# Performance work log

Measured on AMD Instinct MI355X. Metric: run time of the kernel, lower is better.

Reference implementation:

```python
import jax, jax.numpy as jnp
import numpy as np

N_NODES = 100000
N_EDGES = 1600000
IN_DIM = 64
HID_DIM = 128
OUT_DIM = 128


def setup_inputs() -> dict:
    key = jax.random.key(0)
    ks = jax.random.split(key, 12)
    s = 0.05
    return {
        "x": jax.random.normal(ks[0], (N_NODES, IN_DIM), jnp.float32),
        "edge_index": jax.random.randint(ks[1], (2, N_EDGES), 0, N_NODES, jnp.int64),
        "edge_attr": jax.random.uniform(ks[2], (N_EDGES, 2), jnp.float32),
        # conv1 MLP: Linear(IN+2, HID) -> ReLU -> Linear(HID, HID)
        "W11": jax.random.normal(ks[3], (IN_DIM + 2, HID_DIM), jnp.float32) * s,
        "b11": jax.random.normal(ks[4], (HID_DIM,), jnp.float32) * s,
        "W12": jax.random.normal(ks[5], (HID_DIM, HID_DIM), jnp.float32) * s,
        "b12": jax.random.normal(ks[6], (HID_DIM,), jnp.float32) * s,
        # conv2 MLP: Linear(HID+2, OUT) -> ReLU -> Linear(OUT, OUT)
        "W21": jax.random.normal(ks[7], (HID_DIM + 2, OUT_DIM), jnp.float32) * s,
        "b21": jax.random.normal(ks[8], (OUT_DIM,), jnp.float32) * s,
        "W22": jax.random.normal(ks[9], (OUT_DIM, OUT_DIM), jnp.float32) * s,
        "b22": jax.random.normal(ks[10], (OUT_DIM,), jnp.float32) * s,
    }


def _gin_conv(x, edge_index, edge_attr, W1, b1, W2, b2):
    N = x.shape[0]
    loop = jnp.arange(N, dtype=edge_index.dtype)
    src = jnp.concatenate([edge_index[0], loop])  # [E+N] message sources
    dst = jnp.concatenate([edge_index[1], loop])  # [E+N] aggregation targets
    # self-loop edge_attr filled with 1.0 (PyG add_self_loops default)
    ea = jnp.concatenate([edge_attr, jnp.ones((N, edge_attr.shape[1]), edge_attr.dtype)], axis=0)
    m = jnp.concatenate([x[src], ea], axis=-1)  # [E+N, F+2] gather + concat
    h = jnp.dot(jax.nn.relu(jnp.dot(m, W1) + b1), W2) + b2  # edge MLP
    return jax.ops.segment_sum(h, dst, num_segments=N)  # scatter-add aggregate


def reference(x, edge_index, edge_attr, W11, b11, W12, b12, W21, b21, W22, b22):
    h = _gin_conv(x, edge_index, edge_attr, W11, b11, W12, b12)
    h = jax.nn.relu(h)
    return _gin_conv(h, edge_index, edge_attr, W21, b21, W22, b22)
```

## Files before the change

### kernel.cpp

```cpp
#include <hip/hip_runtime.h>


typedef unsigned int uint;
typedef __attribute__((ext_vector_type(8))) short bf16x8;
typedef __attribute__((ext_vector_type(4))) float f32x4;

#define BSHIFT 9
#define BNODES (1 << BSHIFT)

static __device__ __forceinline__ unsigned short f2bf(float f) {
    uint u = __float_as_uint(f);
    uint r = (u + 0x7fffu + ((u >> 16) & 1u)) >> 16;
    return (unsigned short)r;
}


__global__ void wprep_all(const float* __restrict__ W11, const float* __restrict__ W12,
                          const float* __restrict__ W21, const float* __restrict__ W22,
                          unsigned short* Wt11, unsigned short* Wt12,
                          unsigned short* Wt21, unsigned short* Wt22,
                          int* bcnt, int* ptr, int N, int E) {
    int idx = blockIdx.x * 256 + threadIdx.x;
    if (idx < 256) bcnt[idx] = 0;
    if (idx == 0) ptr[N] = E;
    const float* W; unsigned short* Wt; int K; int off;
    if (idx < 64 * 128)        { W = W11; Wt = Wt11; K = 64;  off = idx; }
    else if (idx < 192 * 128)  { W = W12; Wt = Wt12; K = 128; off = idx - 64 * 128; }
    else if (idx < 320 * 128)  { W = W21; Wt = Wt21; K = 128; off = idx - 192 * 128; }
    else if (idx < 448 * 128)  { W = W22; Wt = Wt22; K = 128; off = idx - 320 * 128; }
    else return;
    int k = off >> 7, n = off & 127;
    Wt[n * K + k] = f2bf(W[k * 128 + n]);
}


__global__ __launch_bounds__(512) void bin_kernel(
    const int* __restrict__ src, const int* __restrict__ dst,
    const float* __restrict__ ea, int* __restrict__ bcnt,
    int2* __restrict__ barr, int CAP, int E, int B) {
    __shared__ int hist[256];
    __shared__ int bbase[256];
    __shared__ int gbase[256];
    __shared__ int wtot[4];
    __shared__ int2 sorted[4096];
    __shared__ unsigned char bof[4096];
    const int tileBase = blockIdx.x * 4096;
    int n = E - tileBase; if (n > 4096) n = 4096; if (n <= 0) return;
    const int tid = threadIdx.x;
    const int lane = tid & 63;
    if (tid < 256) hist[tid] = 0;
    __syncthreads();

    int2 ent[8]; int bk[8]; int rk[8];
#pragma unroll
    for (int kk = 0; kk < 8; kk++) {
        int i = kk * 512 + tid;
        bk[kk] = -1;
        if (i < n) {
            int e = tileBase + i;
            int s = src[e], d = dst[e];
            float2 a = reinterpret_cast<const float2*>(ea)[e];
            int b = d >> BSHIFT;
            int dloc = d & (BNODES - 1);
            ent[kk].x = s | (dloc << 17);
            ent[kk].y = (int)((uint)f2bf(a.x) | ((uint)f2bf(a.y) << 16));
            bk[kk] = b;
            rk[kk] = atomicAdd(&hist[b], 1);
        }
    }
    __syncthreads();
    int hv = (tid < 256) ? hist[tid] : 0;
    int inc = hv;
#pragma unroll
    for (int off = 1; off < 64; off <<= 1) {
        int tt = __shfl_up(inc, off, 64);
        if (lane >= off) inc += tt;
    }
    if ((tid >> 6) < 4 && lane == 63) wtot[tid >> 6] = inc;
    __syncthreads();
    if (tid == 0) { int run = 0; for (int i = 0; i < 4; i++) { int tt = wtot[i]; wtot[i] = run; run += tt; } }
    __syncthreads();
    if (tid < 256) bbase[tid] = inc - hv + wtot[tid >> 6];
    if (tid < B && hist[tid] > 0) gbase[tid] = atomicAdd(&bcnt[tid], hist[tid]);
    __syncthreads();
#pragma unroll
    for (int kk = 0; kk < 8; kk++) {
        if (bk[kk] >= 0) {
            int p = bbase[bk[kk]] + rk[kk];
            sorted[p] = ent[kk];
            bof[p] = (unsigned char)bk[kk];
        }
    }
    __syncthreads();
    for (int i = tid; i < n; i += 512) {
        int b = bof[i];
        barr[(long)b * CAP + gbase[b] + (i - bbase[b])] = sorted[i];
    }
}


static __device__ void csr_body(const int2* __restrict__ barr, const int* __restrict__ bcnt,
                                int CAP, int N, int2* __restrict__ csr, int* __restrict__ ptr) {
    __shared__ int hist[BNODES];
    __shared__ int lptr[BNODES];
    __shared__ int wtot[8];
    __shared__ int sbase;
    const int g = blockIdx.x;
    const int tid = threadIdx.x;
    const int lane = tid & 63;
    const int cnt = bcnt[g];
    if (tid == 0) sbase = 0;
    hist[tid] = 0;
    __syncthreads();
    if (tid < g) atomicAdd(&sbase, bcnt[tid]);
    const int2* my = barr + (long)g * CAP;
    for (int i = tid; i < cnt; i += 512)
        atomicAdd(&hist[((uint)my[i].x) >> 17], 1);
    __syncthreads();
    int v = hist[tid];
    int inc = v;
#pragma unroll
    for (int off = 1; off < 64; off <<= 1) {
        int tt = __shfl_up(inc, off, 64);
        if (lane >= off) inc += tt;
    }
    if (lane == 63) wtot[tid >> 6] = inc;
    __syncthreads();
    if (tid == 0) { int run = 0; for (int i = 0; i < 8; i++) { int tt = wtot[i]; wtot[i] = run; run += tt; } }
    __syncthreads();
    const int base = sbase;
    int excl = inc - v + wtot[tid >> 6];
    lptr[tid] = excl;
    int gnode = g * BNODES + tid;
    if (gnode < N) ptr[gnode] = base + excl;
    __syncthreads();
    for (int i = tid; i < cnt; i += 512) {
        int2 e = my[i];
        int pos = base + atomicAdd(&lptr[((uint)e.x) >> 17], 1);
        int2 o; o.x = e.x & 0x1FFFF; o.y = e.y;
        csr[pos] = o;
    }
}


template <int K, bool IN_F32, bool OUT_BF16, bool USE_CNT, bool RELU>
static __device__ __forceinline__ void gemm_body(
    const void* __restrict__ Ain, const unsigned short* __restrict__ Wt,
    const float* __restrict__ bias, const int* __restrict__ ptr,
    void* __restrict__ Cout, int N, int tid, long rowBase) {
    constexpr int KS = K / 32;
    const int wave = tid >> 6;
    const int lane = tid & 63;
    const int m = lane & 15, quad = lane >> 4;

    bf16x8 bfrag[2][KS];
#pragma unroll
    for (int ct = 0; ct < 2; ct++) {
        int col = (wave * 2 + ct) * 16 + m;
#pragma unroll
        for (int ks = 0; ks < KS; ks++)
            bfrag[ct][ks] = *(const bf16x8*)(Wt + (long)col * K + ks * 32 + quad * 8);
    }

#pragma unroll
    for (int rt = 0; rt < 4; rt++) {
        long row = rowBase + rt * 16 + m;
        long rc = row < N ? row : (long)N - 1;
        bf16x8 afrag[KS];
        if (IN_F32) {
            const float* arow = (const float*)Ain + rc * K;
#pragma unroll
            for (int ks = 0; ks < KS; ks++) {
                float4 lo = *(const float4*)(arow + ks * 32 + quad * 8);
                float4 hi = *(const float4*)(arow + ks * 32 + quad * 8 + 4);
                bf16x8 f;
                f[0] = (short)f2bf(lo.x); f[1] = (short)f2bf(lo.y);
                f[2] = (short)f2bf(lo.z); f[3] = (short)f2bf(lo.w);
                f[4] = (short)f2bf(hi.x); f[5] = (short)f2bf(hi.y);
                f[6] = (short)f2bf(hi.z); f[7] = (short)f2bf(hi.w);
                afrag[ks] = f;
            }
        } else {
            const unsigned short* arow = (const unsigned short*)Ain + rc * K;
#pragma unroll
            for (int ks = 0; ks < KS; ks++)
                afrag[ks] = *(const bf16x8*)(arow + ks * 32 + quad * 8);
        }

#pragma unroll
        for (int ct = 0; ct < 2; ct++) {
            f32x4 acc = {0.f, 0.f, 0.f, 0.f};
#pragma unroll
            for (int ks = 0; ks < KS; ks++)
                acc = __builtin_amdgcn_mfma_f32_16x16x32_bf16(afrag[ks], bfrag[ct][ks], acc, 0, 0, 0);

            int col = (wave * 2 + ct) * 16 + m;
            float b = bias[col];
#pragma unroll
            for (int r = 0; r < 4; r++) {
                long orow = rowBase + rt * 16 + quad * 4 + r;
                if (orow < N) {
                    float v = acc[r];
                    if (USE_CNT) v += b * (float)(ptr[orow + 1] - ptr[orow] + 1);
                    else v += b;
                    if (RELU) v = fmaxf(v, 0.f);
                    if (OUT_BF16) ((unsigned short*)Cout)[orow * 128 + col] = f2bf(v);
                    else ((float*)Cout)[orow * 128 + col] = v;
                }
            }
        }
    }
}


__global__ __launch_bounds__(512) void csr_gemm1(
    const int2* __restrict__ barr, const int* __restrict__ bcnt, int CAP, int N,
    int2* __restrict__ csr, int* __restrict__ ptr, int CSRB,
    const float* __restrict__ x, const unsigned short* __restrict__ Wt11,
    const float* __restrict__ b11, unsigned short* __restrict__ A_bf) {
    if ((int)blockIdx.x < CSRB) {
        csr_body(barr, bcnt, CAP, N, csr, ptr);
    } else {
        int bid = blockIdx.x - CSRB;
        int sub = threadIdx.x >> 8;
        gemm_body<64, true, true, false, false>(x, Wt11, b11, nullptr, A_bf, N,
                                                threadIdx.x & 255,
                                                (long)bid * 128 + sub * 64);
    }
}


static __device__ __forceinline__ void gather_lds(
    const uint* __restrict__ Au, const int* __restrict__ ptr,
    const int2* __restrict__ csr, const float* __restrict__ we,
    uint* __restrict__ ts_u, int N, int tid, int rowBase) {
    const int w = tid >> 6;
    const int t = tid & 63;
    const int c = 2 * t;
    const float w0x = we[c], w0y = we[c + 1];
    const float w1x = we[128 + c], w1y = we[128 + c + 1];
    const char* Ab = (const char*)Au;
    const uint t4 = (uint)t * 4u;
#define LD(sidx) (*(const uint*)(Ab + ((((uint)(sidx)) << 8) + t4)))
#define ACC(rv, ev)                                                      \
    {                                                                    \
        float a0 = __uint_as_float(((uint)(ev)) << 16);                  \
        float a1 = __uint_as_float(((uint)(ev)) & 0xffff0000u);          \
        float vx = __uint_as_float((rv) << 16);                          \
        float vy = __uint_as_float((rv) & 0xffff0000u);                  \
        vx = fmaf(a0, w0x, fmaf(a1, w1x, vx));                           \
        vy = fmaf(a0, w0y, fmaf(a1, w1y, vy));                           \
        ax += fmaxf(vx, 0.f);                                            \
        ay += fmaxf(vy, 0.f);                                            \
    }
#define EDGE(i, off)                                                     \
    int2 c##i = csr[k + (off)];                                          \
    uint s##i = (uint)__builtin_amdgcn_readfirstlane(c##i.x);            \
    uint e##i = (uint)__builtin_amdgcn_readfirstlane(c##i.y);

    for (int i = 0; i < 16; i++) {
        int node = rowBase + w * 16 + i;
        if (node >= N) break;

        uint selfv = LD((uint)node);
        float ax = fmaxf(__uint_as_float(selfv << 16) + w0x + w1x, 0.f);
        float ay = fmaxf(__uint_as_float(selfv & 0xffff0000u) + w0y + w1y, 0.f);

        int k   = __builtin_amdgcn_readfirstlane(ptr[node]);
        int end = __builtin_amdgcn_readfirstlane(ptr[node + 1]);

        for (; k + 8 <= end; k += 8) {
            EDGE(0, 0) EDGE(1, 1) EDGE(2, 2) EDGE(3, 3)
            EDGE(4, 4) EDGE(5, 5) EDGE(6, 6) EDGE(7, 7)
            uint r0 = LD(s0); uint r1 = LD(s1); uint r2 = LD(s2); uint r3 = LD(s3);
            uint r4 = LD(s4); uint r5 = LD(s5); uint r6 = LD(s6); uint r7 = LD(s7);
            ACC(r0, e0) ACC(r1, e1) ACC(r2, e2) ACC(r3, e3)
            ACC(r4, e4) ACC(r5, e5) ACC(r6, e6) ACC(r7, e7)
        }
        for (; k + 4 <= end; k += 4) {
            EDGE(0, 0) EDGE(1, 1) EDGE(2, 2) EDGE(3, 3)
            uint r0 = LD(s0); uint r1 = LD(s1); uint r2 = LD(s2); uint r3 = LD(s3);
            ACC(r0, e0) ACC(r1, e1) ACC(r2, e2) ACC(r3, e3)
        }
        for (; k < end; k++) {
            EDGE(0, 0)
            uint r0 = LD(s0);
            ACC(r0, e0)
        }
        ts_u[(w * 16 + i) * 68 + t] = (uint)f2bf(ax) | ((uint)f2bf(ay) << 16);
    }
#undef EDGE
#undef ACC
#undef LD
}


__global__ __launch_bounds__(256, 4) void gather_mid(
    const uint* __restrict__ Au, const int* __restrict__ ptr,
    const int2* __restrict__ csr, const float* __restrict__ we,
    const unsigned short* __restrict__ WtA, const float* __restrict__ biasA,
    const unsigned short* __restrict__ WtB, const float* __restrict__ biasB,
    unsigned short* __restrict__ Cout, int N) {
    __shared__ uint ts_u[64 * 68];
    unsigned short* ts = (unsigned short*)ts_u;
    const int tid = threadIdx.x;
    const int rowBase = blockIdx.x * 64;

    gather_lds(Au, ptr, csr, we, ts_u, N, tid, rowBase);
    __syncthreads();

    const int wave = tid >> 6, lane = tid & 63;
    const int m = lane & 15, quad = lane >> 4;

    bf16x8 bfrag[2][4];
#pragma unroll
    for (int ct = 0; ct < 2; ct++) {
        int col = (wave * 2 + ct) * 16 + m;
#pragma unroll
        for (int ks = 0; ks < 4; ks++)
            bfrag[ct][ks] = *(const bf16x8*)(WtA + (long)col * 128 + ks * 32 + quad * 8);
    }

    f32x4 acc[4][2];
#pragma unroll
    for (int rt = 0; rt < 4; rt++) {
        const unsigned short* lr = ts + (rt * 16 + m) * 136;
        bf16x8 af[4];
#pragma unroll
        for (int ks = 0; ks < 4; ks++)
            af[ks] = *(const bf16x8*)(lr + ks * 32 + quad * 8);
#pragma unroll
        for (int ct = 0; ct < 2; ct++) {
            f32x4 a = {0.f, 0.f, 0.f, 0.f};
#pragma unroll
            for (int ks = 0; ks < 4; ks++)
                a = __builtin_amdgcn_mfma_f32_16x16x32_bf16(af[ks], bfrag[ct][ks], a, 0, 0, 0);
            acc[rt][ct] = a;
        }
    }
    __syncthreads();

#pragma unroll
    for (int rt = 0; rt < 4; rt++) {
        float cntf[4];
#pragma unroll
        for (int r = 0; r < 4; r++) {
            long grow = rowBase + rt * 16 + quad * 4 + r;
            cntf[r] = (grow < N) ? (float)(ptr[grow + 1] - ptr[grow] + 1) : 1.f;
        }
#pragma unroll
        for (int ct = 0; ct < 2; ct++) {
            int col = (wave * 2 + ct) * 16 + m;
            float b = biasA[col];
#pragma unroll
            for (int r = 0; r < 4; r++) {
                int row = rt * 16 + quad * 4 + r;
                ts[row * 136 + col] = f2bf(fmaxf(acc[rt][ct][r] + b * cntf[r], 0.f));
            }
        }
    }
    __syncthreads();

#pragma unroll
    for (int ct = 0; ct < 2; ct++) {
        int col = (wave * 2 + ct) * 16 + m;
#pragma unroll
        for (int ks = 0; ks < 4; ks++)
            bfrag[ct][ks] = *(const bf16x8*)(WtB + (long)col * 128 + ks * 32 + quad * 8);
    }
#pragma unroll
    for (int rt = 0; rt < 4; rt++) {
        const unsigned short* lr = ts + (rt * 16 + m) * 136;
        bf16x8 af[4];
#pragma unroll
        for (int ks = 0; ks < 4; ks++)
            af[ks] = *(const bf16x8*)(lr + ks * 32 + quad * 8);
#pragma unroll
        for (int ct = 0; ct < 2; ct++) {
            f32x4 a = {0.f, 0.f, 0.f, 0.f};
#pragma unroll
            for (int ks = 0; ks < 4; ks++)
                a = __builtin_amdgcn_mfma_f32_16x16x32_bf16(af[ks], bfrag[ct][ks], a, 0, 0, 0);
            int col = (wave * 2 + ct) * 16 + m;
            float b = biasB[col];
#pragma unroll
            for (int r = 0; r < 4; r++) {
                long grow = rowBase + rt * 16 + quad * 4 + r;
                if (grow < N) Cout[grow * 128 + col] = f2bf(a[r] + b);
            }
        }
    }
}


__global__ __launch_bounds__(256, 4) void gather_out(
    const uint* __restrict__ Au, const int* __restrict__ ptr,
    const int2* __restrict__ csr, const float* __restrict__ we,
    const unsigned short* __restrict__ Wt, const float* __restrict__ bias,
    float* __restrict__ out, int N) {
    __shared__ uint ts_u[64 * 68];
    unsigned short* ts = (unsigned short*)ts_u;
    const int tid = threadIdx.x;
    const int rowBase = blockIdx.x * 64;

    gather_lds(Au, ptr, csr, we, ts_u, N, tid, rowBase);
    __syncthreads();

    const int wave = tid >> 6, lane = tid & 63;
    const int m = lane & 15, quad = lane >> 4;

    bf16x8 bfrag[2][4];
#pragma unroll
    for (int ct = 0; ct < 2; ct++) {
        int col = (wave * 2 + ct) * 16 + m;
#pragma unroll
        for (int ks = 0; ks < 4; ks++)
            bfrag[ct][ks] = *(const bf16x8*)(Wt + (long)col * 128 + ks * 32 + quad * 8);
    }

#pragma unroll
    for (int rt = 0; rt < 4; rt++) {
        const unsigned short* lr = ts + (rt * 16 + m) * 136;
        bf16x8 af[4];
#pragma unroll
        for (int ks = 0; ks < 4; ks++)
            af[ks] = *(const bf16x8*)(lr + ks * 32 + quad * 8);
#pragma unroll
        for (int ct = 0; ct < 2; ct++) {
            f32x4 a = {0.f, 0.f, 0.f, 0.f};
#pragma unroll
            for (int ks = 0; ks < 4; ks++)
                a = __builtin_amdgcn_mfma_f32_16x16x32_bf16(af[ks], bfrag[ct][ks], a, 0, 0, 0);
            int col = (wave * 2 + ct) * 16 + m;
            float b = bias[col];
#pragma unroll
            for (int r = 0; r < 4; r++) {
                long grow = rowBase + rt * 16 + quad * 4 + r;
                if (grow < N) {
                    float cnt = (float)(ptr[grow + 1] - ptr[grow] + 1);
                    out[grow * 128 + col] = a[r] + b * cnt;
                }
            }
        }
    }
}


extern "C" void kernel_launch(void* const* d_in, const int* in_sizes, int n_in,
                              void* d_out, int out_size, void* d_ws, size_t ws_size,
                              hipStream_t stream) {
    const float* x   = (const float*)d_in[0];
    const int*   ei  = (const int*)d_in[1];
    const float* ea  = (const float*)d_in[2];
    const float* W11 = (const float*)d_in[3];
    const float* b11 = (const float*)d_in[4];
    const float* W12 = (const float*)d_in[5];
    const float* b12 = (const float*)d_in[6];
    const float* W21 = (const float*)d_in[7];
    const float* b21 = (const float*)d_in[8];
    const float* W22 = (const float*)d_in[9];
    const float* b22 = (const float*)d_in[10];
    float* out = (float*)d_out;

    const int N = in_sizes[0] / 64;
    const int E = in_sizes[1] / 2;
    const int* src = ei;
    const int* dst = ei + E;

    const int B = (N + BNODES - 1) >> BSHIFT;
    const int CAP = E / B + 4096;

    char* p = (char*)d_ws;
    unsigned short* A_bf = (unsigned short*)p;  p += (size_t)N * 128 * 2;
    unsigned short* A2_bf = (unsigned short*)p;
    int2* barr = (int2*)A2_bf;                  p += (size_t)N * 128 * 2;
    int2* csr  = (int2*)p;                      p += (size_t)E * 8;
    int* ptr   = (int*)p;                       p += (size_t)(N + 1) * 4;
    int* bcnt  = (int*)p;                       p += 256 * 4;
    unsigned short* Wt11 = (unsigned short*)p;  p += (size_t)64 * 128 * 2;
    unsigned short* Wt12 = (unsigned short*)p;  p += (size_t)128 * 128 * 2;
    unsigned short* Wt21 = (unsigned short*)p;  p += (size_t)128 * 128 * 2;
    unsigned short* Wt22 = (unsigned short*)p;

    const int binBlocks = (E + 4095) / 4096;
    const int tileBlocks = (N + 63) / 64;
    const int g1Tiles = (N + 127) / 128;

    wprep_all<<<224, 256, 0, stream>>>(W11, W12, W21, W22,
                                       Wt11, Wt12, Wt21, Wt22,
                                       bcnt, ptr, N, E);
    bin_kernel<<<binBlocks, 512, 0, stream>>>(src, dst, ea, bcnt, barr, CAP, E, B);
    csr_gemm1<<<B + g1Tiles, 512, 0, stream>>>(barr, bcnt, CAP, N, csr, ptr, B,
                                               x, Wt11, b11, A_bf);
    gather_mid<<<tileBlocks, 256, 0, stream>>>((const uint*)A_bf, ptr, csr,
                                               W11 + 64 * 128, Wt12, b12, Wt21, b21,
                                               A2_bf, N);
    gather_out<<<tileBlocks, 256, 0, stream>>>((const uint*)A2_bf, ptr, csr,
                                               W21 + 128 * 128, Wt22, b22, out, N);
}
```

Before: 347.3 us.

## Fuse weight prep into binning, interleave two-node gathers, drop occupancy hints

The weight-transpose kernel is merged into the binning kernel as extra blocks, and the bcnt zeroing moves to a hipMemsetAsync. The gather loop now processes two nodes at once with interleaved 4-edge batches, which raises memory-level parallelism, though the 8-edge unroll is gone. The __launch_bounds__ occupancy hint of 4 is removed from the gather kernels. The output kernel hoists the degree counts out of the column loop and uses nontemporal stores. Dropping the occupancy hint may raise register use and lower the number of resident waves.

```diff
diff --git a/kernel.cpp b/kernel.cpp
--- a/kernel.cpp
+++ b/kernel.cpp
@@ -2,52 +2,55 @@
 
 
 typedef unsigned int uint;
+typedef unsigned short ushort;
 typedef __attribute__((ext_vector_type(8))) short bf16x8;
 typedef __attribute__((ext_vector_type(4))) float f32x4;
 
 #define BSHIFT 9
 #define BNODES (1 << BSHIFT)
 
-static __device__ __forceinline__ unsigned short f2bf(float f) {
+static __device__ __forceinline__ ushort f2bf(float f) {
     uint u = __float_as_uint(f);
     uint r = (u + 0x7fffu + ((u >> 16) & 1u)) >> 16;
-    return (unsigned short)r;
-}
-
-
-__global__ void wprep_all(const float* __restrict__ W11, const float* __restrict__ W12,
-                          const float* __restrict__ W21, const float* __restrict__ W22,
-                          unsigned short* Wt11, unsigned short* Wt12,
-                          unsigned short* Wt21, unsigned short* Wt22,
-                          int* bcnt, int* ptr, int N, int E) {
-    int idx = blockIdx.x * 256 + threadIdx.x;
-    if (idx < 256) bcnt[idx] = 0;
-    if (idx == 0) ptr[N] = E;
-    const float* W; unsigned short* Wt; int K; int off;
-    if (idx < 64 * 128)        { W = W11; Wt = Wt11; K = 64;  off = idx; }
-    else if (idx < 192 * 128)  { W = W12; Wt = Wt12; K = 128; off = idx - 64 * 128; }
-    else if (idx < 320 * 128)  { W = W21; Wt = Wt21; K = 128; off = idx - 192 * 128; }
-    else if (idx < 448 * 128)  { W = W22; Wt = Wt22; K = 128; off = idx - 320 * 128; }
-    else return;
-    int k = off >> 7, n = off & 127;
-    Wt[n * K + k] = f2bf(W[k * 128 + n]);
-}
-
-
-__global__ __launch_bounds__(512) void bin_kernel(
+    return (ushort)r;
+}
+static __device__ __forceinline__ int rfl(int v) { return __builtin_amdgcn_readfirstlane(v); }
+
+
+__global__ __launch_bounds__(512) void wprep_bin(
+    const float* __restrict__ W11, const float* __restrict__ W12,
+    const float* __restrict__ W21, const float* __restrict__ W22,
+    ushort* Wt11, ushort* Wt12, ushort* Wt21, ushort* Wt22,
     const int* __restrict__ src, const int* __restrict__ dst,
     const float* __restrict__ ea, int* __restrict__ bcnt,
-    int2* __restrict__ barr, int CAP, int E, int B) {
+    int2* __restrict__ barr, int CAP, int N, int E, int B, int WB,
+    int* __restrict__ ptr) {
     __shared__ int hist[256];
     __shared__ int bbase[256];
     __shared__ int gbase[256];
     __shared__ int wtot[4];
     __shared__ int2 sorted[4096];
     __shared__ unsigned char bof[4096];
-    const int tileBase = blockIdx.x * 4096;
-    int n = E - tileBase; if (n > 4096) n = 4096; if (n <= 0) return;
     const int tid = threadIdx.x;
     const int lane = tid & 63;
+
+    if ((int)blockIdx.x < WB) {
+        int idx = blockIdx.x * 512 + tid;
+        if (idx == 0) ptr[N] = E;
+        if (idx < 448 * 128) {
+            const float* W; ushort* Wt; int K; int off;
+            if (idx < 64 * 128)        { W = W11; Wt = Wt11; K = 64;  off = idx; }
+            else if (idx < 192 * 128)  { W = W12; Wt = Wt12; K = 128; off = idx - 64 * 128; }
+            else if (idx < 320 * 128)  { W = W21; Wt = Wt21; K = 128; off = idx - 192 * 128; }
+            else                       { W = W22; Wt = Wt22; K = 128; off = idx - 320 * 128; }
+            int k = off >> 7, n = off & 127;
+            Wt[n * K + k] = f2bf(W[k * 128 + n]);
+        }
+        return;
+    }
+
+    const int tileBase = ((int)blockIdx.x - WB) * 4096;
+    int n = E - tileBase; if (n > 4096) n = 4096; if (n <= 0) return;
     if (tid < 256) hist[tid] = 0;
     __syncthreads();
 
@@ -81,7 +84,7 @@
     if (tid == 0) { int run = 0; for (int i = 0; i < 4; i++) { int tt = wtot[i]; wtot[i] = run; run += tt; } }
     __syncthreads();
     if (tid < 256) bbase[tid] = inc - hv + wtot[tid >> 6];
-    if (tid < B && hist[tid] > 0) gbase[tid] = atomicAdd(&bcnt[tid], hist[tid]);
+    if (tid < B && hv > 0) gbase[tid] = atomicAdd(&bcnt[tid], hv);
     __syncthreads();
 #pragma unroll
     for (int kk = 0; kk < 8; kk++) {
@@ -143,9 +146,9 @@
 }
 
 
-template <int K, bool IN_F32, bool OUT_BF16, bool USE_CNT, bool RELU>
+template <int K, bool IN_F32, bool OUT_BF16, bool USE_CNT>
 static __device__ __forceinline__ void gemm_body(
-    const void* __restrict__ Ain, const unsigned short* __restrict__ Wt,
+    const void* __restrict__ Ain, const ushort* __restrict__ Wt,
     const float* __restrict__ bias, const int* __restrict__ ptr,
     void* __restrict__ Cout, int N, int tid, long rowBase) {
     constexpr int KS = K / 32;
@@ -181,7 +184,7 @@
                 afrag[ks] = f;
             }
         } else {
-            const unsigned short* arow = (const unsigned short*)Ain + rc * K;
+            const ushort* arow = (const ushort*)Ain + rc * K;
 #pragma unroll
             for (int ks = 0; ks < KS; ks++)
                 afrag[ks] = *(const bf16x8*)(arow + ks * 32 + quad * 8);
@@ -203,8 +206,7 @@
                     float v = acc[r];
                     if (USE_CNT) v += b * (float)(ptr[orow + 1] - ptr[orow] + 1);
                     else v += b;
-                    if (RELU) v = fmaxf(v, 0.f);
-                    if (OUT_BF16) ((unsigned short*)Cout)[orow * 128 + col] = f2bf(v);
+                    if (OUT_BF16) ((ushort*)Cout)[orow * 128 + col] = f2bf(v);
                     else ((float*)Cout)[orow * 128 + col] = v;
                 }
             }
@@ -216,19 +218,58 @@
 __global__ __launch_bounds__(512) void csr_gemm1(
     const int2* __restrict__ barr, const int* __restrict__ bcnt, int CAP, int N,
     int2* __restrict__ csr, int* __restrict__ ptr, int CSRB,
-    const float* __restrict__ x, const unsigned short* __restrict__ Wt11,
-    const float* __restrict__ b11, unsigned short* __restrict__ A_bf) {
+    const float* __restrict__ x, const ushort* __restrict__ Wt11,
+    const float* __restrict__ b11, ushort* __restrict__ A_bf) {
     if ((int)blockIdx.x < CSRB) {
         csr_body(barr, bcnt, CAP, N, csr, ptr);
     } else {
         int bid = blockIdx.x - CSRB;
         int sub = threadIdx.x >> 8;
-        gemm_body<64, true, true, false, false>(x, Wt11, b11, nullptr, A_bf, N,
-                                                threadIdx.x & 255,
-                                                (long)bid * 128 + sub * 64);
-    }
-}
-
+        gemm_body<64, true, true, false>(x, Wt11, b11, nullptr, A_bf, N,
+                                         threadIdx.x & 255,
+                                         (long)bid * 128 + sub * 64);
+    }
+}
+
+
+static __device__ __forceinline__ uint ldrow(const char* Ab, uint t4, uint sidx) {
+    return *(const uint*)(Ab + ((sidx << 8) + t4));
+}
+static __device__ __forceinline__ void accum_edge(
+    uint rv, uint ev, float w0x, float w0y, float w1x, float w1y,
+    float& ax, float& ay) {
+    float a0 = __uint_as_float(ev << 16);
+    float a1 = __uint_as_float(ev & 0xffff0000u);
+    float vx = __uint_as_float(rv << 16);
+    float vy = __uint_as_float(rv & 0xffff0000u);
+    vx = fmaf(a0, w0x, fmaf(a1, w1x, vx));
+    vy = fmaf(a0, w0y, fmaf(a1, w1y, vy));
+    ax += fmaxf(vx, 0.f);
+    ay += fmaxf(vy, 0.f);
+}
+static __device__ __forceinline__ void drain_node(
+    const char* Ab, uint t4, const int2* __restrict__ csr, int k, int end,
+    float w0x, float w0y, float w1x, float w1y, float& ax, float& ay) {
+    for (; k + 4 <= end; k += 4) {
+        int2 c0 = csr[k], c1 = csr[k + 1], c2 = csr[k + 2], c3 = csr[k + 3];
+        uint s0 = (uint)rfl(c0.x), e0 = (uint)rfl(c0.y);
+        uint s1 = (uint)rfl(c1.x), e1 = (uint)rfl(c1.y);
+        uint s2 = (uint)rfl(c2.x), e2 = (uint)rfl(c2.y);
+        uint s3 = (uint)rfl(c3.x), e3 = (uint)rfl(c3.y);
+        uint r0 = ldrow(Ab, t4, s0), r1 = ldrow(Ab, t4, s1);
+        uint r2 = ldrow(Ab, t4, s2), r3 = ldrow(Ab, t4, s3);
+        accum_edge(r0, e0, w0x, w0y, w1x, w1y, ax, ay);
+        accum_edge(r1, e1, w0x, w0y, w1x, w1y, ax, ay);
+        accum_edge(r2, e2, w0x, w0y, w1x, w1y, ax, ay);
+        accum_edge(r3, e3, w0x, w0y, w1x, w1y, ax, ay);
+    }
+    for (; k < end; k++) {
+        int2 c0 = csr[k];
+        uint s0 = (uint)rfl(c0.x), e0 = (uint)rfl(c0.y);
+        uint r0 = ldrow(Ab, t4, s0);
+        accum_edge(r0, e0, w0x, w0y, w1x, w1y, ax, ay);
+    }
+}
 
 static __device__ __forceinline__ void gather_lds(
     const uint* __restrict__ Au, const int* __restrict__ ptr,
@@ -241,68 +282,72 @@
     const float w1x = we[128 + c], w1y = we[128 + c + 1];
     const char* Ab = (const char*)Au;
     const uint t4 = (uint)t * 4u;
-#define LD(sidx) (*(const uint*)(Ab + ((((uint)(sidx)) << 8) + t4)))
-#define ACC(rv, ev)                                                      \
-    {                                                                    \
-        float a0 = __uint_as_float(((uint)(ev)) << 16);                  \
-        float a1 = __uint_as_float(((uint)(ev)) & 0xffff0000u);          \
-        float vx = __uint_as_float((rv) << 16);                          \
-        float vy = __uint_as_float((rv) & 0xffff0000u);                  \
-        vx = fmaf(a0, w0x, fmaf(a1, w1x, vx));                           \
-        vy = fmaf(a0, w0y, fmaf(a1, w1y, vy));                           \
-        ax += fmaxf(vx, 0.f);                                            \
-        ay += fmaxf(vy, 0.f);                                            \
-    }
-#define EDGE(i, off)                                                     \
-    int2 c##i = csr[k + (off)];                                          \
-    uint s##i = (uint)__builtin_amdgcn_readfirstlane(c##i.x);            \
-    uint e##i = (uint)__builtin_amdgcn_readfirstlane(c##i.y);
-
-    for (int i = 0; i < 16; i++) {
-        int node = rowBase + w * 16 + i;
-        if (node >= N) break;
-
-        uint selfv = LD((uint)node);
-        float ax = fmaxf(__uint_as_float(selfv << 16) + w0x + w1x, 0.f);
-        float ay = fmaxf(__uint_as_float(selfv & 0xffff0000u) + w0y + w1y, 0.f);
-
-        int k   = __builtin_amdgcn_readfirstlane(ptr[node]);
-        int end = __builtin_amdgcn_readfirstlane(ptr[node + 1]);
-
-        for (; k + 8 <= end; k += 8) {
-            EDGE(0, 0) EDGE(1, 1) EDGE(2, 2) EDGE(3, 3)
-            EDGE(4, 4) EDGE(5, 5) EDGE(6, 6) EDGE(7, 7)
-            uint r0 = LD(s0); uint r1 = LD(s1); uint r2 = LD(s2); uint r3 = LD(s3);
-            uint r4 = LD(s4); uint r5 = LD(s5); uint r6 = LD(s6); uint r7 = LD(s7);
-            ACC(r0, e0) ACC(r1, e1) ACC(r2, e2) ACC(r3, e3)
-            ACC(r4, e4) ACC(r5, e5) ACC(r6, e6) ACC(r7, e7)
-        }
-        for (; k + 4 <= end; k += 4) {
-            EDGE(0, 0) EDGE(1, 1) EDGE(2, 2) EDGE(3, 3)
-            uint r0 = LD(s0); uint r1 = LD(s1); uint r2 = LD(s2); uint r3 = LD(s3);
-            ACC(r0, e0) ACC(r1, e1) ACC(r2, e2) ACC(r3, e3)
-        }
-        for (; k < end; k++) {
-            EDGE(0, 0)
-            uint r0 = LD(s0);
-            ACC(r0, e0)
-        }
-        ts_u[(w * 16 + i) * 68 + t] = (uint)f2bf(ax) | ((uint)f2bf(ay) << 16);
-    }
-#undef EDGE
-#undef ACC
-#undef LD
-}
-
-
-__global__ __launch_bounds__(256, 4) void gather_mid(
+    const int nodeBase = rowBase + w * 16;
+    if (nodeBase >= N) return;
+    int kNext = rfl(ptr[nodeBase]);
+
+    for (int i = 0; i < 16; i += 2) {
+        const int n0 = nodeBase + i;
+        if (n0 >= N) break;
+        const int n1 = n0 + 1;
+        const bool h1 = (n1 < N);
+        int k0 = kNext;
+        int e0 = rfl(ptr[n0 + 1]);
+        int k1 = e0, e1 = e0;
+        if (h1) { e1 = rfl(ptr[n1 + 1]); kNext = e1; }
+
+        uint sv0 = ldrow(Ab, t4, (uint)n0);
+        float ax0 = fmaxf(__uint_as_float(sv0 << 16) + w0x + w1x, 0.f);
+        float ay0 = fmaxf(__uint_as_float(sv0 & 0xffff0000u) + w0y + w1y, 0.f);
+        float ax1 = 0.f, ay1 = 0.f;
+        if (h1) {
+            uint sv1 = ldrow(Ab, t4, (uint)n1);
+            ax1 = fmaxf(__uint_as_float(sv1 << 16) + w0x + w1x, 0.f);
+            ay1 = fmaxf(__uint_as_float(sv1 & 0xffff0000u) + w0y + w1y, 0.f);
+        }
+        while (k0 + 4 <= e0 && k1 + 4 <= e1) {
+            int2 ca0 = csr[k0], ca1 = csr[k0 + 1], ca2 = csr[k0 + 2], ca3 = csr[k0 + 3];
+            int2 cb0 = csr[k1], cb1 = csr[k1 + 1], cb2 = csr[k1 + 2], cb3 = csr[k1 + 3];
+            uint sa0 = (uint)rfl(ca0.x), ea0 = (uint)rfl(ca0.y);
+            uint sa1 = (uint)rfl(ca1.x), ea1 = (uint)rfl(ca1.y);
+            uint sa2 = (uint)rfl(ca2.x), ea2 = (uint)rfl(ca2.y);
+            uint sa3 = (uint)rfl(ca3.x), ea3 = (uint)rfl(ca3.y);
+            uint sb0 = (uint)rfl(cb0.x), eb0 = (uint)rfl(cb0.y);
+            uint sb1 = (uint)rfl(cb1.x), eb1 = (uint)rfl(cb1.y);
+            uint sb2 = (uint)rfl(cb2.x), eb2 = (uint)rfl(cb2.y);
+            uint sb3 = (uint)rfl(cb3.x), eb3 = (uint)rfl(cb3.y);
+            uint ra0 = ldrow(Ab, t4, sa0), ra1 = ldrow(Ab, t4, sa1);
+            uint ra2 = ldrow(Ab, t4, sa2), ra3 = ldrow(Ab, t4, sa3);
+            uint rb0 = ldrow(Ab, t4, sb0), rb1 = ldrow(Ab, t4, sb1);
+            uint rb2 = ldrow(Ab, t4, sb2), rb3 = ldrow(Ab, t4, sb3);
+            accum_edge(ra0, ea0, w0x, w0y, w1x, w1y, ax0, ay0);
+            accum_edge(ra1, ea1, w0x, w0y, w1x, w1y, ax0, ay0);
+            accum_edge(ra2, ea2, w0x, w0y, w1x, w1y, ax0, ay0);
+            accum_edge(ra3, ea3, w0x, w0y, w1x, w1y, ax0, ay0);
+            accum_edge(rb0, eb0, w0x, w0y, w1x, w1y, ax1, ay1);
+            accum_edge(rb1, eb1, w0x, w0y, w1x, w1y, ax1, ay1);
+            accum_edge(rb2, eb2, w0x, w0y, w1x, w1y, ax1, ay1);
+            accum_edge(rb3, eb3, w0x, w0y, w1x, w1y, ax1, ay1);
+            k0 += 4; k1 += 4;
+        }
+        drain_node(Ab, t4, csr, k0, e0, w0x, w0y, w1x, w1y, ax0, ay0);
+        ts_u[(w * 16 + i) * 68 + t] = (uint)f2bf(ax0) | ((uint)f2bf(ay0) << 16);
+        if (h1) {
+            drain_node(Ab, t4, csr, k1, e1, w0x, w0y, w1x, w1y, ax1, ay1);
+            ts_u[(w * 16 + i + 1) * 68 + t] = (uint)f2bf(ax1) | ((uint)f2bf(ay1) << 16);
+        }
+    }
+}
+
+
+__global__ __launch_bounds__(256) void gather_mid(
     const uint* __restrict__ Au, const int* __restrict__ ptr,
     const int2* __restrict__ csr, const float* __restrict__ we,
-    const unsigned short* __restrict__ WtA, const float* __restrict__ biasA,
-    const unsigned short* __restrict__ WtB, const float* __restrict__ biasB,
-    unsigned short* __restrict__ Cout, int N) {
+    const ushort* __restrict__ WtA, const float* __restrict__ biasA,
+    const ushort* __restrict__ WtB, const float* __restrict__ biasB,
+    ushort* __restrict__ Cout, int N) {
     __shared__ uint ts_u[64 * 68];
-    unsigned short* ts = (unsigned short*)ts_u;
+    ushort* ts = (ushort*)ts_u;
     const int tid = threadIdx.x;
     const int rowBase = blockIdx.x * 64;
 
@@ -324,7 +369,7 @@
     f32x4 acc[4][2];
 #pragma unroll
     for (int rt = 0; rt < 4; rt++) {
-        const unsigned short* lr = ts + (rt * 16 + m) * 136;
+        const ushort* lr = ts + (rt * 16 + m) * 136;
         bf16x8 af[4];
 #pragma unroll
         for (int ks = 0; ks < 4; ks++)
@@ -370,7 +415,7 @@
     }
 #pragma unroll
     for (int rt = 0; rt < 4; rt++) {
-        const unsigned short* lr = ts + (rt * 16 + m) * 136;
+        const ushort* lr = ts + (rt * 16 + m) * 136;
         bf16x8 af[4];
 #pragma unroll
         for (int ks = 0; ks < 4; ks++)
@@ -393,13 +438,13 @@
 }
 
 
-__global__ __launch_bounds__(256, 4) void gather_out(
+__global__ __launch_bounds__(256) void gather_out(
     const uint* __restrict__ Au, const int* __restrict__ ptr,
     const int2* __restrict__ csr, const float* __restrict__ we,
-    const unsigned short* __restrict__ Wt, const float* __restrict__ bias,
+    const ushort* __restrict__ Wt, const float* __restrict__ bias,
     float* __restrict__ out, int N) {
     __shared__ uint ts_u[64 * 68];
-    unsigned short* ts = (unsigned short*)ts_u;
+    ushort* ts = (ushort*)ts_u;
     const int tid = threadIdx.x;
     const int rowBase = blockIdx.x * 64;
 
@@ -420,11 +465,17 @@
 
 #pragma unroll
     for (int rt = 0; rt < 4; rt++) {
-        const unsigned short* lr = ts + (rt * 16 + m) * 136;
+        const ushort* lr = ts + (rt * 16 + m) * 136;
         bf16x8 af[4];
 #pragma unroll
         for (int ks = 0; ks < 4; ks++)
             af[ks] = *(const bf16x8*)(lr + ks * 32 + quad * 8);
+        float cntf[4];
+#pragma unroll
+        for (int r = 0; r < 4; r++) {
+            long grow = rowBase + rt * 16 + quad * 4 + r;
+            cntf[r] = (grow < N) ? (float)(ptr[grow + 1] - ptr[grow] + 1) : 1.f;
+        }
 #pragma unroll
         for (int ct = 0; ct < 2; ct++) {
             f32x4 a = {0.f, 0.f, 0.f, 0.f};
@@ -436,10 +487,9 @@
 #pragma unroll
             for (int r = 0; r < 4; r++) {
                 long grow = rowBase + rt * 16 + quad * 4 + r;
-                if (grow < N) {
-                    float cnt = (float)(ptr[grow + 1] - ptr[grow] + 1);
-                    out[grow * 128 + col] = a[r] + b * cnt;
-                }
+                if (grow < N)
+                    __builtin_nontemporal_store(a[r] + b * cntf[r],
+                                                &out[grow * 128 + col]);
             }
         }
     }
@@ -471,25 +521,26 @@
     const int CAP = E / B + 4096;
 
     char* p = (char*)d_ws;
-    unsigned short* A_bf = (unsigned short*)p;  p += (size_t)N * 128 * 2;
-    unsigned short* A2_bf = (unsigned short*)p;
-    int2* barr = (int2*)A2_bf;                  p += (size_t)N * 128 * 2;
-    int2* csr  = (int2*)p;                      p += (size_t)E * 8;
-    int* ptr   = (int*)p;                       p += (size_t)(N + 1) * 4;
-    int* bcnt  = (int*)p;                       p += 256 * 4;
-    unsigned short* Wt11 = (unsigned short*)p;  p += (size_t)64 * 128 * 2;
-    unsigned short* Wt12 = (unsigned short*)p;  p += (size_t)128 * 128 * 2;
-    unsigned short* Wt21 = (unsigned short*)p;  p += (size_t)128 * 128 * 2;
-    unsigned short* Wt22 = (unsigned short*)p;
-
+    ushort* A_bf = (ushort*)p;        p += (size_t)N * 128 * 2;
+    ushort* A2_bf = (ushort*)p;
+    int2* barr = (int2*)A2_bf;        p += (size_t)N * 128 * 2;
+    int2* csr  = (int2*)p;            p += (size_t)E * 8;
+    int* ptr   = (int*)p;             p += (size_t)(N + 1) * 4;
+    int* bcnt  = (int*)p;             p += 256 * 4;
+    ushort* Wt11 = (ushort*)p;        p += (size_t)64 * 128 * 2;
+    ushort* Wt12 = (ushort*)p;        p += (size_t)128 * 128 * 2;
+    ushort* Wt21 = (ushort*)p;        p += (size_t)128 * 128 * 2;
+    ushort* Wt22 = (ushort*)p;
+
+    const int WB = (448 * 128 + 511) / 512;
     const int binBlocks = (E + 4095) / 4096;
     const int tileBlocks = (N + 63) / 64;
     const int g1Tiles = (N + 127) / 128;
 
-    wprep_all<<<224, 256, 0, stream>>>(W11, W12, W21, W22,
-                                       Wt11, Wt12, Wt21, Wt22,
-                                       bcnt, ptr, N, E);
-    bin_kernel<<<binBlocks, 512, 0, stream>>>(src, dst, ea, bcnt, barr, CAP, E, B);
+    hipMemsetAsync(bcnt, 0, 256 * sizeof(int), stream);
+    wprep_bin<<<WB + binBlocks, 512, 0, stream>>>(
+        W11, W12, W21, W22, Wt11, Wt12, Wt21, Wt22,
+        src, dst, ea, bcnt, barr, CAP, N, E, B, WB, ptr);
     csr_gemm1<<<B + g1Tiles, 512, 0, stream>>>(barr, bcnt, CAP, N, csr, ptr, B,
                                                x, Wt11, b11, A_bf);
     gather_mid<<<tileBlocks, 256, 0, stream>>>((const uint*)A_bf, ptr, csr,
```

New measurement: 464.6 us. 1.34x slower.
